# Kernel tuning notes

Hardware: AMD Instinct MI355X
Metric: run time of the kernel (lower is better)

## Reference

```python
import jax, jax.numpy as jnp
import numpy as np

T, B, D, H, DH = 2048, 2, 1024, 16, 64


def _rel_shift(x):
    # x: (Q, R, B, H) -- standard Transformer-XL relative shift via pad/reshape
    Q, R = x.shape[0], x.shape[1]
    zero_pad = jnp.zeros((Q, 1) + x.shape[2:], dtype=x.dtype)
    xp = jnp.concatenate([zero_pad, x], axis=1)          # (Q, R+1, B, H)
    xp = xp.reshape((R + 1, Q) + x.shape[2:])            # (R+1, Q, B, H)
    return xp[1:].reshape(x.shape)                       # (Q, R, B, H)


def setup_inputs() -> dict:
    key = jax.random.key(0)
    ks = jax.random.split(key, 7)
    w = jax.random.normal(ks[0], (T, B, D), dtype=jnp.float32)
    r = jax.random.normal(ks[1], (T, D), dtype=jnp.float32)
    w_qkv = jax.random.normal(ks[2], (3 * H * DH, D), dtype=jnp.float32) * 0.02
    w_r = jax.random.normal(ks[3], (H * DH, D), dtype=jnp.float32) * 0.02
    w_o = jax.random.normal(ks[4], (D, H * DH), dtype=jnp.float32) * 0.02
    r_r_bias = jax.random.normal(ks[5], (H, DH), dtype=jnp.float32) * 0.02
    attn_mask = jax.random.uniform(ks[6], (T, B)) < 0.1
    return {"w": w, "r": r, "w_qkv": w_qkv, "w_r": w_r, "w_o": w_o,
            "r_r_bias": r_r_bias, "attn_mask": attn_mask}


def reference(w, r, w_qkv, w_r, w_o, r_r_bias, attn_mask):
    qlen, bsz, d_model = w.shape
    n_head, d_head = r_r_bias.shape
    rlen = r.shape[0]
    scale = 1.0 / d_head ** 0.5

    heads = jnp.einsum('tbd,ed->tbe', w, w_qkv)           # (T, B, 3*H*DH)
    q, k, v = jnp.split(heads, 3, axis=-1)
    q = q.reshape(qlen, bsz, n_head, d_head)
    k = k.reshape(qlen, bsz, n_head, d_head)
    v = v.reshape(qlen, bsz, n_head, d_head)
    r_head_k = jnp.einsum('rd,ed->re', r, w_r).reshape(rlen, n_head, d_head)

    # NOTE: source uses r_r_bias for BOTH content and position biases
    rq = q + r_r_bias[None, None]                         # (Q, B, H, DH)
    AC = jnp.einsum('qbhd,kbhd->bhqk', rq, k)             # content scores
    BD = jnp.einsum('qbhd,rhd->bhqr', rq, r_head_k)       # position scores

    BD = jnp.transpose(BD, (2, 3, 0, 1))                  # (Q, R, B, H)
    BD = _rel_shift(BD)
    BD = jnp.transpose(BD, (2, 3, 0, 1))                  # (B, H, Q, R)
    BD = BD[:, :, :, :qlen]                               # klen == qlen

    score = (AC + BD) * scale                             # (B, H, Q, K)
    # key-padding mask (K, B) -> broadcast (B, 1, 1, K)
    score = jnp.where(attn_mask.T[:, None, None, :], -jnp.inf, score)

    prob = jax.nn.softmax(score.astype(jnp.float32), axis=-1).astype(score.dtype)
    attn_vec = jnp.einsum('bhqk,kbhd->qbhd', prob, v).reshape(qlen, bsz, n_head * d_head)
    out = jnp.einsum('qbe,de->qbd', attn_vec, w_o)        # (Q, B, D)
    return out, prob
```

## Files before the change

kernel.cpp:

```cpp
#include <hip/hip_runtime.h>
#include <hip/hip_bf16.h>
#include <cstdint>
#include <cstddef>

#define TLEN 2048
#define NB 2
#define DMODEL 1024
#define NH 16
#define NDH 64

typedef unsigned short ushortT;
typedef short bf16x8 __attribute__((ext_vector_type(8)));
typedef float f32x16 __attribute__((ext_vector_type(16)));

__device__ __forceinline__ ushortT f2bf(float f) {
  union { float f; unsigned int u; } x{f};
  unsigned int r = x.u + 0x7fff + ((x.u >> 16) & 1);
  return (ushortT)(r >> 16);
}
__device__ __forceinline__ unsigned int pk2(float lo, float hi) {
  return ((unsigned int)f2bf(hi) << 16) | (unsigned int)f2bf(lo);
}
__device__ __forceinline__ float bf2f(ushortT u) {
  union { unsigned int u; float f; } x;
  x.u = ((unsigned int)u) << 16;
  return x.f;
}

__device__ __forceinline__ void gld_lds16(const void* g, void* l) {
  __builtin_amdgcn_global_load_lds(
      (const __attribute__((address_space(1))) unsigned int*)g,
      (__attribute__((address_space(3))) unsigned int*)l, 16, 0, 0);
}


__global__ __launch_bounds__(256) void cvt_bf16(const float* __restrict__ in,
                                                ushortT* __restrict__ out, int n4) {
  int i = blockIdx.x * 256 + threadIdx.x;
  if (i < n4) {
    float4 v = reinterpret_cast<const float4*>(in)[i];
    ushort4 o;
    o.x = f2bf(v.x); o.y = f2bf(v.y); o.z = f2bf(v.z); o.w = f2bf(v.w);
    reinterpret_cast<ushort4*>(out)[i] = o;
  }
}

__global__ __launch_bounds__(256) void cvt_mask(const int* __restrict__ mask,
                                                float* __restrict__ mfl) {
  int j = blockIdx.x * 256 + threadIdx.x;
  if (j < TLEN) {
    mfl[j]        = mask[j * NB]     ? 0.f : 1.f;
    mfl[TLEN + j] = mask[j * NB + 1] ? 0.f : 1.f;
  }
}

__global__ __launch_bounds__(256) void zero_rkext(ushortT* __restrict__ rkE) {
  int i = threadIdx.x;
  int h = i >> 4, c = i & 15;
  ushort4 z; z.x = 0; z.y = 0; z.z = 0; z.w = 0;
  *reinterpret_cast<ushort4*>(rkE + ((size_t)h * 4096 + 2048) * NDH + c * 4) = z;
}


template <typename Epi>
__global__ __launch_bounds__(256) void gemm_bf16(const ushortT* __restrict__ A,
                                                 const ushortT* __restrict__ B,
                                                 int K, Epi epi) {
  __shared__ ushortT Al[128 * 64];
  __shared__ ushortT Bl[128 * 64];
  const int tid = threadIdx.x;
  const int lane = tid & 63;
  const int wv = tid >> 6;
  const int wm = wv >> 1, wn = wv & 1;
  const int m0 = blockIdx.y * 128;
  const int n0 = blockIdx.x * 128;
  const int r32 = lane & 31;
  const int hh = lane >> 5;

  f32x16 acc[2][2];
#pragma unroll
  for (int i = 0; i < 2; ++i)
#pragma unroll
    for (int j = 0; j < 2; ++j)
#pragma unroll
      for (int e = 0; e < 16; ++e) acc[i][j][e] = 0.f;

  for (int k0 = 0; k0 < K; k0 += 64) {
#pragma unroll
    for (int it = 0; it < 4; ++it) {
      int idx = it * 256 + tid;
      int r = idx >> 3, c = idx & 7;
      int gcol = k0 + ((c ^ (r & 7)) << 3);
      gld_lds16(A + (size_t)(m0 + r) * K + gcol, Al + idx * 8);
      gld_lds16(B + (size_t)(n0 + r) * K + gcol, Bl + idx * 8);
    }
    asm volatile("s_waitcnt vmcnt(0)");
    __syncthreads();
#pragma unroll
    for (int kc = 0; kc < 4; ++kc) {
      int lc = kc * 2 + hh;
      bf16x8 af[2], bfr[2];
#pragma unroll
      for (int f = 0; f < 2; ++f) {
        int ar = wm * 64 + f * 32 + r32;
        af[f] = *(const bf16x8*)(Al + ar * 64 + ((lc ^ (ar & 7)) << 3));
        int br = wn * 64 + f * 32 + r32;
        bfr[f] = *(const bf16x8*)(Bl + br * 64 + ((lc ^ (br & 7)) << 3));
      }
#pragma unroll
      for (int i = 0; i < 2; ++i)
#pragma unroll
        for (int j = 0; j < 2; ++j)
          acc[i][j] = __builtin_amdgcn_mfma_f32_32x32x16_bf16(af[i], bfr[j],
                                                              acc[i][j], 0, 0, 0);
    }
    __syncthreads();
  }

#pragma unroll
  for (int i = 0; i < 2; ++i)
#pragma unroll
    for (int j = 0; j < 2; ++j)
#pragma unroll
      for (int rg = 0; rg < 16; ++rg) {
        int m = m0 + wm * 64 + i * 32 + (rg & 3) + 8 * (rg >> 2) + 4 * hh;
        int n = n0 + wn * 64 + j * 32 + r32;
        epi.store(m, n, acc[i][j][rg]);
      }
}

struct EpiQKV {
  ushortT* qb; ushortT* kb; ushortT* vtb; const float* bias;
  __device__ void store(int m, int n, float val) const {
    int t = m >> 1, b = m & 1;
    int which = n >> 10;
    int h = (n >> 6) & (NH - 1);
    int dh = n & (NDH - 1);
    int bh = b * NH + h;
    if (which == 0)
      qb[((size_t)bh * TLEN + t) * NDH + dh] = f2bf(val + bias[(h << 6) | dh]);
    else if (which == 1)
      kb[((size_t)bh * TLEN + t) * NDH + dh] = f2bf(val);
    else
      vtb[((size_t)bh * NDH + dh) * TLEN + t] = f2bf(val);
  }
};

struct EpiRK {
  ushortT* rkE;
  __device__ void store(int m, int n, float val) const {
    int h = n >> 6, dh = n & 63;
    ushortT v = f2bf(val);
    rkE[((size_t)h * 4096 + m) * NDH + dh] = v;
    if (m <= 2046)
      rkE[((size_t)h * 4096 + m + 2049) * NDH + dh] = v;
  }
};

struct EpiOut {
  float* out;
  __device__ void store(int m, int n, float val) const {
    out[(size_t)m * DMODEL + n] = val;
  }
};


__global__ __launch_bounds__(128) void attn_fast(
    const ushortT* __restrict__ qb, const ushortT* __restrict__ kb,
    const ushortT* __restrict__ vtb, const ushortT* __restrict__ rkE,
    const float* __restrict__ mfl, unsigned int* __restrict__ S,
    float* __restrict__ linv_g, ushortT* __restrict__ av_bf) {
  __shared__ float W[2][64][32];
  __shared__ ushortT KT[2048];
  __shared__ ushortT VT[2048];
  __shared__ ushortT RK[6144];

  const int bh = blockIdx.y;
  const int b = bh >> 4, h = bh & 15;
  const int t = threadIdx.x >> 6;
  const int lane = threadIdx.x & 63;
  const int ql = lane & 31;
  const int hh = lane >> 5;
  const int Q0 = blockIdx.x * 64;
  const int q0 = Q0 + 32 * t;
  const int qg = q0 + ql;

  const ushortT* Qbh = qb + (size_t)bh * TLEN * NDH;
  const ushortT* Kbh = kb + (size_t)bh * TLEN * NDH;
  const ushortT* Vbh = vtb + (size_t)bh * NDH * TLEN;
  const ushortT* Rh  = rkE + (size_t)h * 4096 * NDH;
  const float* mflb  = mfl + (size_t)b * TLEN;
  unsigned int* Sb   = S + (size_t)bh * (TLEN / 2) * TLEN;
  float (*Wp)[32] = W[t];

  bf16x8 Qf[4], Qs[4];
  {
    int r2 = min(qg + 1, TLEN - 1);
#pragma unroll
    for (int c = 0; c < 4; ++c) {
      Qf[c] = *(const bf16x8*)(Qbh + (size_t)qg * NDH + c * 16 + hh * 8);
      Qs[c] = *(const bf16x8*)(Qbh + (size_t)r2 * NDH + c * 16 + hh * 8);
    }
  }

  f32x16 pacc0, pacc1;
#pragma unroll
  for (int i = 0; i < 16; ++i) { pacc0[i] = 0.f; pacc1[i] = 0.f; }
  float l_acc = 0.f;

  for (int j0 = 0; j0 < TLEN; j0 += 32) {
    __syncthreads();
    const int U = 1984 + j0 - Q0;
#pragma unroll
    for (int i = 0; i < 6; ++i) {
      int ci = (t * 6 + i) * 64 + lane;
      int row = ci >> 3, c = ci & 7;
      gld_lds16(Rh + (size_t)(U + row) * NDH + ((c ^ (row & 7)) << 3), RK + ci * 8);
    }
#pragma unroll
    for (int i = 0; i < 2; ++i) {
      int ci = (t * 2 + i) * 64 + lane;
      int row = ci >> 3, c = ci & 7;
      gld_lds16(Kbh + (size_t)(j0 + row) * NDH + ((c ^ (row & 7)) << 3), KT + ci * 8);
      int d = ci >> 2, c2 = ci & 3;
      gld_lds16(Vbh + (size_t)d * TLEN + j0 + ((c2 ^ (d & 3)) << 3), VT + ci * 8);
    }
    float4 mf4[4];
#pragma unroll
    for (int g = 0; g < 4; ++g)
      mf4[g] = *(const float4*)(mflb + j0 + 8 * g + 4 * hh);
    asm volatile("s_waitcnt vmcnt(0)");
    __syncthreads();

    const bool t0w1 = (j0 <= q0);
    const bool t1w1 = (j0 < q0);
    const int R1 = 32 * (1 - t) + ql;
    const int R2 = R1 + 32;

    f32x16 facc;
#pragma unroll
    for (int i = 0; i < 16; ++i) facc[i] = 0.f;
    __builtin_amdgcn_s_setprio(1);
#pragma unroll
    for (int c = 0; c < 4; ++c) {
      bf16x8 a = *(const bf16x8*)(RK + R1 * NDH + (((2 * c + hh) ^ (R1 & 7)) << 3));
      facc = __builtin_amdgcn_mfma_f32_32x32x16_bf16(a, t0w1 ? Qf[c] : Qs[c], facc, 0, 0, 0);
    }
    __builtin_amdgcn_s_setprio(0);
#pragma unroll
    for (int r = 0; r < 16; ++r)
      Wp[(r & 3) + 8 * (r >> 2) + 4 * hh][ql] = facc[r];

#pragma unroll
    for (int i = 0; i < 16; ++i) facc[i] = 0.f;
    __builtin_amdgcn_s_setprio(1);
#pragma unroll
    for (int c = 0; c < 4; ++c) {
      bf16x8 a = *(const bf16x8*)(RK + R2 * NDH + (((2 * c + hh) ^ (R2 & 7)) << 3));
      facc = __builtin_amdgcn_mfma_f32_32x32x16_bf16(a, t1w1 ? Qf[c] : Qs[c], facc, 0, 0, 0);
    }
    __builtin_amdgcn_s_setprio(0);
#pragma unroll
    for (int r = 0; r < 16; ++r)
      Wp[32 + (r & 3) + 8 * (r >> 2) + 4 * hh][ql] = facc[r];

    f32x16 cacc;
#pragma unroll
    for (int i = 0; i < 16; ++i) cacc[i] = 0.f;
    __builtin_amdgcn_s_setprio(1);
#pragma unroll
    for (int c = 0; c < 4; ++c) {
      bf16x8 a = *(const bf16x8*)(KT + ql * NDH + (((2 * c + hh) ^ (ql & 7)) << 3));
      cacc = __builtin_amdgcn_mfma_f32_32x32x16_bf16(a, Qf[c], cacc, 0, 0, 0);
    }
    __builtin_amdgcn_s_setprio(0);

    float p[16];
#pragma unroll
    for (int r = 0; r < 16; ++r) {
      int jrow = (r & 3) + 8 * (r >> 2) + 4 * hh;
      float bd = Wp[jrow - ql + 31][ql];
      float sc = (cacc[r] + bd) * 0.125f;
      float mv = (&mf4[r >> 2].x)[r & 3];
      float pv = mv * __expf(sc);
      p[r] = pv;
      l_acc += pv;
    }

    unsigned int u[8];
#pragma unroll
    for (int i = 0; i < 8; ++i) u[i] = pk2(p[2 * i], p[2 * i + 1]);

#pragma unroll
    for (int i = 0; i < 8; ++i) {
      int r = 2 * i;
      int jrow = (r & 3) + 8 * (r >> 2) + 4 * hh;
      Sb[(size_t)((j0 + jrow) >> 1) * TLEN + qg] = u[i];
    }

#pragma unroll
    for (int kh = 0; kh < 2; ++kh) {
      unsigned int t0 = (unsigned int)__shfl_xor((int)u[4 * kh + 0], 32);
      unsigned int t1 = (unsigned int)__shfl_xor((int)u[4 * kh + 1], 32);
      unsigned int t2 = (unsigned int)__shfl_xor((int)u[4 * kh + 2], 32);
      unsigned int t3 = (unsigned int)__shfl_xor((int)u[4 * kh + 3], 32);
      unsigned int fr[4];
      fr[0] = hh ? t2 : u[4 * kh + 0];
      fr[1] = hh ? t3 : u[4 * kh + 1];
      fr[2] = hh ? u[4 * kh + 2] : t0;
      fr[3] = hh ? u[4 * kh + 3] : t1;
      bf16x8 pa = *reinterpret_cast<bf16x8*>(fr);
      bf16x8 v0 = *(const bf16x8*)(VT + ql * 32 + (((2 * kh + hh) ^ (ql & 3)) << 3));
      bf16x8 v1 = *(const bf16x8*)(VT + (32 + ql) * 32 + (((2 * kh + hh) ^ (ql & 3)) << 3));
      __builtin_amdgcn_s_setprio(1);
      pacc0 = __builtin_amdgcn_mfma_f32_32x32x16_bf16(pa, v0, pacc0, 0, 0, 0);
      pacc1 = __builtin_amdgcn_mfma_f32_32x32x16_bf16(pa, v1, pacc1, 0, 0, 0);
      __builtin_amdgcn_s_setprio(0);
    }
  }

  float lt = l_acc + __shfl_xor(l_acc, 32);
  if (lane < 32) linv_g[(size_t)bh * TLEN + qg] = 1.0f / lt;
  float inv = 1.0f / lt;
#pragma unroll
  for (int r = 0; r < 16; ++r) {
    int qrow = (r & 3) + 8 * (r >> 2) + 4 * hh;
    float iv = __shfl(inv, qrow);
    size_t aoff = ((size_t)(q0 + qrow) * NB + b) * DMODEL + h * NDH;
    av_bf[aoff + ql] = f2bf(pacc0[r] * iv);
    av_bf[aoff + 32 + ql] = f2bf(pacc1[r] * iv);
  }
}


__global__ __launch_bounds__(256) void rescale_t(const unsigned int* __restrict__ S,
                                                 const float* __restrict__ linv_g,
                                                 float* __restrict__ prob) {
  __shared__ unsigned int lds[64][65];
  __shared__ float liv[64];
  const int qt = blockIdx.x;
  const int jt = blockIdx.y;
  const int bh = blockIdx.z;
  const int t = threadIdx.x;

  const unsigned int* Sb = S + ((size_t)bh * (TLEN / 2) + jt * 64) * TLEN + qt * 64;
  {
    int row = t >> 2, c0 = (t & 3) * 16;
#pragma unroll
    for (int k = 0; k < 4; ++k) {
      uint4 v = *reinterpret_cast<const uint4*>(Sb + (size_t)row * TLEN + c0 + k * 4);
      lds[row][c0 + k * 4 + 0] = v.x;
      lds[row][c0 + k * 4 + 1] = v.y;
      lds[row][c0 + k * 4 + 2] = v.z;
      lds[row][c0 + k * 4 + 3] = v.w;
    }
  }
  if (t < 64) liv[t] = linv_g[(size_t)bh * TLEN + qt * 64 + t];
  __syncthreads();

  float* P = prob + ((size_t)bh * TLEN + qt * 64) * TLEN + jt * 128;
#pragma unroll
  for (int k = 0; k < 8; ++k) {
    int idx = k * 256 + t;
    int row = idx >> 5, c4 = idx & 31;
    unsigned int u0 = lds[c4 * 2][row];
    unsigned int u1 = lds[c4 * 2 + 1][row];
    float iv = liv[row];
    float4 o;
    o.x = bf2f((ushortT)(u0 & 0xffff)) * iv;
    o.y = bf2f((ushortT)(u0 >> 16)) * iv;
    o.z = bf2f((ushortT)(u1 & 0xffff)) * iv;
    o.w = bf2f((ushortT)(u1 >> 16)) * iv;
    *reinterpret_cast<float4*>(P + (size_t)row * TLEN + c4 * 4) = o;
  }
}


__global__ __launch_bounds__(256) void attn_fused(
    const ushortT* __restrict__ qb, const ushortT* __restrict__ kb,
    const ushortT* __restrict__ vtb, const ushortT* __restrict__ rkE,
    const float* __restrict__ mfl, float* __restrict__ prob,
    ushortT* __restrict__ av_bf) {
  __shared__ float W[4][64][32];
  __shared__ float sl[4][32];
  __shared__ float linv[64];

  const int bh = blockIdx.y;
  const int b = bh >> 4, h = bh & 15;
  const int wv = threadIdx.x >> 6;
  const int lane = threadIdx.x & 63;
  const int ql = lane & 31;
  const int hh = lane >> 5;
  const int qtile = wv & 1;
  const int jh = wv >> 1;
  const int q0 = blockIdx.x * 64 + qtile * 32;
  const int qg = q0 + ql;

  const ushortT* Qbh = qb + (size_t)bh * TLEN * NDH;
  const ushortT* Kbh = kb + (size_t)bh * TLEN * NDH;
  const ushortT* Vbh = vtb + (size_t)bh * NDH * TLEN;
  const ushortT* Rh  = rkE + (size_t)h * 4096 * NDH;
  const float* mflb  = mfl + (size_t)b * TLEN;
  float (*Wp)[32] = W[wv];

  bf16x8 Qf[4], Qs[4];
  {
    int r2 = min(qg + 1, TLEN - 1);
#pragma unroll
    for (int c = 0; c < 4; ++c) {
      Qf[c] = *(const bf16x8*)(Qbh + (size_t)qg * NDH + c * 16 + hh * 8);
      Qs[c] = *(const bf16x8*)(Qbh + (size_t)r2 * NDH + c * 16 + hh * 8);
    }
  }

  f32x16 pacc0, pacc1;
#pragma unroll
  for (int i = 0; i < 16; ++i) { pacc0[i] = 0.f; pacc1[i] = 0.f; }
  float l_acc = 0.f;

  ushortT* pbrow = (ushortT*)prob + ((size_t)bh * TLEN + qg) * 4096 + 2048;

  const int jbeg = jh * (TLEN / 2);
  const int jend = jbeg + (TLEN / 2);
  for (int j0 = jbeg; j0 < jend; j0 += 32) {
    const int base_t = 2016 + j0 - q0;
    const bool t0w1 = (j0 <= q0);
    const bool t1w1 = (j0 < q0);

    const ushortT* s0 = Rh + (size_t)(base_t + ql) * NDH + hh * 8;
    const ushortT* s1 = Rh + (size_t)(base_t + 32 + ql) * NDH + hh * 8;
    const ushortT* sk = Kbh + (size_t)(j0 + ql) * NDH + hh * 8;
    const ushortT* vrow0 = Vbh + (size_t)ql * TLEN + j0 + 8 * hh;
    const ushortT* vrow1 = Vbh + (size_t)(32 + ql) * TLEN + j0 + 8 * hh;
    bf16x8 rk0[4], rk1[4], kk[4];
#pragma unroll
    for (int c = 0; c < 4; ++c) {
      rk0[c] = *(const bf16x8*)(s0 + c * 16);
      rk1[c] = *(const bf16x8*)(s1 + c * 16);
      kk[c]  = *(const bf16x8*)(sk + c * 16);
    }
    bf16x8 v00 = *(const bf16x8*)(vrow0);
    bf16x8 v01 = *(const bf16x8*)(vrow0 + 16);
    bf16x8 v10 = *(const bf16x8*)(vrow1);
    bf16x8 v11 = *(const bf16x8*)(vrow1 + 16);
    float4 mf4[4];
#pragma unroll
    for (int g = 0; g < 4; ++g)
      mf4[g] = *(const float4*)(mflb + j0 + 8 * g + 4 * hh);

    f32x16 facc;
#pragma unroll
    for (int i = 0; i < 16; ++i) facc[i] = 0.f;
    __builtin_amdgcn_s_setprio(1);
#pragma unroll
    for (int c = 0; c < 4; ++c)
      facc = __builtin_amdgcn_mfma_f32_32x32x16_bf16(rk0[c], t0w1 ? Qf[c] : Qs[c], facc, 0, 0, 0);
    __builtin_amdgcn_s_setprio(0);
#pragma unroll
    for (int r = 0; r < 16; ++r)
      Wp[(r & 3) + 8 * (r >> 2) + 4 * hh][ql] = facc[r];

#pragma unroll
    for (int i = 0; i < 16; ++i) facc[i] = 0.f;
    __builtin_amdgcn_s_setprio(1);
#pragma unroll
    for (int c = 0; c < 4; ++c)
      facc = __builtin_amdgcn_mfma_f32_32x32x16_bf16(rk1[c], t1w1 ? Qf[c] : Qs[c], facc, 0, 0, 0);
    __builtin_amdgcn_s_setprio(0);
#pragma unroll
    for (int r = 0; r < 16; ++r)
      Wp[32 + (r & 3) + 8 * (r >> 2) + 4 * hh][ql] = facc[r];

    f32x16 cacc;
#pragma unroll
    for (int i = 0; i < 16; ++i) cacc[i] = 0.f;
    __builtin_amdgcn_s_setprio(1);
#pragma unroll
    for (int c = 0; c < 4; ++c)
      cacc = __builtin_amdgcn_mfma_f32_32x32x16_bf16(kk[c], Qf[c], cacc, 0, 0, 0);
    __builtin_amdgcn_s_setprio(0);

    float p[16];
#pragma unroll
    for (int r = 0; r < 16; ++r) {
      int jrow = (r & 3) + 8 * (r >> 2) + 4 * hh;
      float bd = Wp[jrow - ql + 31][ql];
      float sc = (cacc[r] + bd) * 0.125f;
      float mv = (&mf4[r >> 2].x)[r & 3];
      float pv = mv * __expf(sc);
      p[r] = pv;
      l_acc += pv;
    }

#pragma unroll
    for (int g = 0; g < 4; ++g) {
      uint2 st;
      st.x = pk2(p[4 * g + 0], p[4 * g + 1]);
      st.y = pk2(p[4 * g + 2], p[4 * g + 3]);
      *reinterpret_cast<uint2*>(pbrow + j0 + 8 * g + 4 * hh) = st;
    }

#pragma unroll
    for (int kh = 0; kh < 2; ++kh) {
      unsigned int u0 = pk2(p[8 * kh + 0], p[8 * kh + 1]);
      unsigned int u1 = pk2(p[8 * kh + 2], p[8 * kh + 3]);
      unsigned int u2 = pk2(p[8 * kh + 4], p[8 * kh + 5]);
      unsigned int u3 = pk2(p[8 * kh + 6], p[8 * kh + 7]);
      unsigned int t0 = (unsigned int)__shfl_xor((int)u0, 32);
      unsigned int t1 = (unsigned int)__shfl_xor((int)u1, 32);
      unsigned int t2 = (unsigned int)__shfl_xor((int)u2, 32);
      unsigned int t3 = (unsigned int)__shfl_xor((int)u3, 32);
      unsigned int fr[4];
      fr[0] = hh ? t2 : u0;
      fr[1] = hh ? t3 : u1;
      fr[2] = hh ? u2 : t0;
      fr[3] = hh ? u3 : t1;
      bf16x8 pa = *reinterpret_cast<bf16x8*>(fr);
      __builtin_amdgcn_s_setprio(1);
      pacc0 = __builtin_amdgcn_mfma_f32_32x32x16_bf16(pa, kh ? v01 : v00, pacc0, 0, 0, 0);
      pacc1 = __builtin_amdgcn_mfma_f32_32x32x16_bf16(pa, kh ? v11 : v10, pacc1, 0, 0, 0);
      __builtin_amdgcn_s_setprio(0);
    }
  }

#pragma unroll
  for (int r = 0; r < 16; ++r) {
    int qrow = (r & 3) + 8 * (r >> 2) + 4 * hh;
    Wp[qrow][ql] = pacc0[r];
    Wp[32 + qrow][ql] = pacc1[r];
  }
  float lh = l_acc + __shfl_xor(l_acc, 32);
  if (lane < 32) sl[wv][ql] = lh;
  __syncthreads();

  if (wv < 2) {
    if (lane < 32) {
      float lt = sl[wv][ql] + sl[wv + 2][ql];
      linv[wv * 32 + ql] = 1.0f / lt;
    }
#pragma unroll
    for (int r = 0; r < 16; ++r) {
      int qrow = (r & 3) + 8 * (r >> 2) + 4 * hh;
      float lt = sl[wv][qrow] + sl[wv + 2][qrow];
      float iv = 1.0f / lt;
      float s0v = W[wv][qrow][ql] + W[wv + 2][qrow][ql];
      float s1v = W[wv][32 + qrow][ql] + W[wv + 2][32 + qrow][ql];
      size_t aoff = ((size_t)(q0 + qrow) * NB + b) * DMODEL + h * NDH;
      av_bf[aoff + ql] = f2bf(s0v * iv);
      av_bf[aoff + 32 + ql] = f2bf(s1v * iv);
    }
  }
  __syncthreads();

  const ushortT* probus = (const ushortT*)prob;
  const int lr = lane >> 4;
  const int cg = lane & 15;
  for (int s = 0; s < 8; ++s) {
    const int rloc = qtile * 32 + s * 4 + lr;
    const int rowg = blockIdx.x * 64 + rloc;
    const size_t ub = ((size_t)bh * TLEN + rowg) * 4096 + 2048 + jh * 1024 + cg * 8;
    const size_t fb = ((size_t)bh * TLEN + rowg) * 2048 + jh * 1024 + cg * 8;
    uint4 a[8];
#pragma unroll
    for (int k = 0; k < 8; ++k)
      a[k] = *reinterpret_cast<const uint4*>(probus + ub + k * 128);
    const float iv = linv[rloc];
    __syncthreads();
#pragma unroll
    for (int k = 0; k < 8; ++k) {
      float4 o0, o1;
      o0.x = bf2f((ushortT)(a[k].x & 0xffff)) * iv;
      o0.y = bf2f((ushortT)(a[k].x >> 16)) * iv;
      o0.z = bf2f((ushortT)(a[k].y & 0xffff)) * iv;
      o0.w = bf2f((ushortT)(a[k].y >> 16)) * iv;
      o1.x = bf2f((ushortT)(a[k].z & 0xffff)) * iv;
      o1.y = bf2f((ushortT)(a[k].z >> 16)) * iv;
      o1.z = bf2f((ushortT)(a[k].w & 0xffff)) * iv;
      o1.w = bf2f((ushortT)(a[k].w >> 16)) * iv;
      *reinterpret_cast<float4*>(prob + fb + k * 128) = o0;
      *reinterpret_cast<float4*>(prob + fb + k * 128 + 4) = o1;
    }
  }
}


extern "C" void kernel_launch(void* const* d_in, const int* in_sizes, int n_in,
                              void* d_out, int out_size, void* d_ws, size_t ws_size,
                              hipStream_t stream) {
  const float* w      = (const float*)d_in[0];
  const float* r      = (const float*)d_in[1];
  const float* w_qkv  = (const float*)d_in[2];
  const float* w_r    = (const float*)d_in[3];
  const float* w_o    = (const float*)d_in[4];
  const float* bias   = (const float*)d_in[5];
  const int* mask     = (const int*)d_in[6];

  float* out  = (float*)d_out;
  float* prob = out + (size_t)TLEN * NB * DMODEL;

  const size_t SZ = (size_t)NB * NH * TLEN * NDH;
  ushortT* w_bf    = (ushortT*)d_ws;
  ushortT* wqkv_bf = w_bf + (size_t)4096 * 1024;
  ushortT* r_bf    = wqkv_bf + (size_t)3072 * 1024;
  ushortT* wr_bf   = r_bf + (size_t)2048 * 1024;
  ushortT* wo_bf   = wr_bf + (size_t)1024 * 1024;
  ushortT* q_bf    = wo_bf + (size_t)1024 * 1024;
  ushortT* k_bf    = q_bf + SZ;
  ushortT* vt_bf   = k_bf + SZ;
  ushortT* rkE_bf  = vt_bf + SZ;
  ushortT* av_bf   = rkE_bf + (size_t)NH * 4096 * NDH;
  float* mfl       = (float*)(av_bf + SZ);
  float* linv_g    = mfl + (size_t)NB * TLEN;
  unsigned int* S  = (unsigned int*)(linv_g + (size_t)NB * NH * TLEN);
  const size_t need = (size_t)((char*)(S + (size_t)NB * NH * (TLEN / 2) * TLEN) -
                               (char*)d_ws);
  const bool fast = ws_size >= need;

  cvt_bf16<<<4096, 256, 0, stream>>>(w, w_bf, 4096 * 1024 / 4);
  cvt_bf16<<<3072, 256, 0, stream>>>(w_qkv, wqkv_bf, 3072 * 1024 / 4);
  cvt_bf16<<<2048, 256, 0, stream>>>(r, r_bf, 2048 * 1024 / 4);
  cvt_bf16<<<1024, 256, 0, stream>>>(w_r, wr_bf, 1024 * 1024 / 4);
  cvt_bf16<<<1024, 256, 0, stream>>>(w_o, wo_bf, 1024 * 1024 / 4);
  cvt_mask<<<8, 256, 0, stream>>>(mask, mfl);
  zero_rkext<<<1, 256, 0, stream>>>(rkE_bf);

  EpiQKV e1{q_bf, k_bf, vt_bf, bias};
  gemm_bf16<EpiQKV><<<dim3(3072 / 128, 4096 / 128), 256, 0, stream>>>(w_bf, wqkv_bf, DMODEL, e1);
  EpiRK e2{rkE_bf};
  gemm_bf16<EpiRK><<<dim3(1024 / 128, 2048 / 128), 256, 0, stream>>>(r_bf, wr_bf, DMODEL, e2);

  if (fast) {
    attn_fast<<<dim3(32, 32), 128, 0, stream>>>(q_bf, k_bf, vt_bf, rkE_bf,
                                                mfl, S, linv_g, av_bf);
    rescale_t<<<dim3(32, 16, 32), 256, 0, stream>>>(S, linv_g, prob);
  } else {
    attn_fused<<<dim3(32, 32), 256, 0, stream>>>(q_bf, k_bf, vt_bf, rkE_bf,
                                                 mfl, prob, av_bf);
  }

  EpiOut e5{out};
  gemm_bf16<EpiOut><<<dim3(1024 / 128, 4096 / 128), 256, 0, stream>>>(av_bf, wo_bf, DMODEL, e5);
}
```

Baseline: 471.3 us.

## Prefetch next attention tile during compute and merge conversion kernels into one launch

The attention loop now pulls all LDS operands for the current tile into registers, then issues the async global-to-LDS loads for the next tile before running the MFMAs, so load latency overlaps compute. It uses a single LDS buffer and relies on barriers and a partial vmcnt wait to keep the two phases apart. Separately, the five bf16 conversion kernels plus the mask and zero-fill kernels are folded into one launch to cut launch overhead. The register-held operands raise register pressure, and a wrong wait count could race on the shared buffers.

New measurement: 445.4 us (median of 2 runs). 5.5% less time.

```diff
diff --git a/kernel.cpp b/kernel.cpp
--- a/kernel.cpp
+++ b/kernel.cpp
@@ -34,31 +34,43 @@
 }
 
 
-__global__ __launch_bounds__(256) void cvt_bf16(const float* __restrict__ in,
-                                                ushortT* __restrict__ out, int n4) {
-  int i = blockIdx.x * 256 + threadIdx.x;
-  if (i < n4) {
-    float4 v = reinterpret_cast<const float4*>(in)[i];
-    ushort4 o;
-    o.x = f2bf(v.x); o.y = f2bf(v.y); o.z = f2bf(v.z); o.w = f2bf(v.w);
-    reinterpret_cast<ushort4*>(out)[i] = o;
-  }
-}
-
-__global__ __launch_bounds__(256) void cvt_mask(const int* __restrict__ mask,
-                                                float* __restrict__ mfl) {
-  int j = blockIdx.x * 256 + threadIdx.x;
-  if (j < TLEN) {
-    mfl[j]        = mask[j * NB]     ? 0.f : 1.f;
-    mfl[TLEN + j] = mask[j * NB + 1] ? 0.f : 1.f;
-  }
-}
-
-__global__ __launch_bounds__(256) void zero_rkext(ushortT* __restrict__ rkE) {
-  int i = threadIdx.x;
-  int h = i >> 4, c = i & 15;
-  ushort4 z; z.x = 0; z.y = 0; z.z = 0; z.w = 0;
-  *reinterpret_cast<ushort4*>(rkE + ((size_t)h * 4096 + 2048) * NDH + c * 4) = z;
+__global__ __launch_bounds__(256) void cvt_all(
+    const float* __restrict__ w, const float* __restrict__ wqkv,
+    const float* __restrict__ r, const float* __restrict__ wr,
+    const float* __restrict__ wo, ushortT* __restrict__ w_bf,
+    ushortT* __restrict__ wqkv_bf, ushortT* __restrict__ r_bf,
+    ushortT* __restrict__ wr_bf, ushortT* __restrict__ wo_bf,
+    const int* __restrict__ mask, float* __restrict__ mfl,
+    ushortT* __restrict__ rkE) {
+  const size_t N0 = 1048576, N1 = N0 + 786432, N2 = N1 + 524288,
+               N3 = N2 + 262144, N4 = N3 + 262144;
+  size_t i = (size_t)blockIdx.x * 256 + threadIdx.x;
+  const float* src; ushortT* dst; size_t off;
+  if (i < N0)      { src = w;    dst = w_bf;    off = i; }
+  else if (i < N1) { src = wqkv; dst = wqkv_bf; off = i - N0; }
+  else if (i < N2) { src = r;    dst = r_bf;    off = i - N1; }
+  else if (i < N3) { src = wr;   dst = wr_bf;   off = i - N2; }
+  else if (i < N4) { src = wo;   dst = wo_bf;   off = i - N3; }
+  else {
+    size_t k = i - N4;
+    if (k < 512) {
+      int j = (int)k * 4;
+#pragma unroll
+      for (int s = 0; s < 4; ++s) {
+        mfl[j + s]        = mask[(size_t)(j + s) * NB]     ? 0.f : 1.f;
+        mfl[TLEN + j + s] = mask[(size_t)(j + s) * NB + 1] ? 0.f : 1.f;
+      }
+    } else if (k < 512 + 256) {
+      int ii = (int)k - 512; int h = ii >> 4, c = ii & 15;
+      ushort4 z; z.x = 0; z.y = 0; z.z = 0; z.w = 0;
+      *reinterpret_cast<ushort4*>(rkE + ((size_t)h * 4096 + 2048) * NDH + c * 4) = z;
+    }
+    return;
+  }
+  float4 v = reinterpret_cast<const float4*>(src)[off];
+  ushort4 o;
+  o.x = f2bf(v.x); o.y = f2bf(v.y); o.z = f2bf(v.z); o.w = f2bf(v.w);
+  reinterpret_cast<ushort4*>(dst)[off] = o;
 }
 
 
@@ -193,23 +205,7 @@
   unsigned int* Sb   = S + (size_t)bh * (TLEN / 2) * TLEN;
   float (*Wp)[32] = W[t];
 
-  bf16x8 Qf[4], Qs[4];
-  {
-    int r2 = min(qg + 1, TLEN - 1);
-#pragma unroll
-    for (int c = 0; c < 4; ++c) {
-      Qf[c] = *(const bf16x8*)(Qbh + (size_t)qg * NDH + c * 16 + hh * 8);
-      Qs[c] = *(const bf16x8*)(Qbh + (size_t)r2 * NDH + c * 16 + hh * 8);
-    }
-  }
-
-  f32x16 pacc0, pacc1;
-#pragma unroll
-  for (int i = 0; i < 16; ++i) { pacc0[i] = 0.f; pacc1[i] = 0.f; }
-  float l_acc = 0.f;
-
-  for (int j0 = 0; j0 < TLEN; j0 += 32) {
-    __syncthreads();
+  auto STAGE = [&](int j0) {
     const int U = 1984 + j0 - Q0;
 #pragma unroll
     for (int i = 0; i < 6; ++i) {
@@ -225,27 +221,63 @@
       int d = ci >> 2, c2 = ci & 3;
       gld_lds16(Vbh + (size_t)d * TLEN + j0 + ((c2 ^ (d & 3)) << 3), VT + ci * 8);
     }
+  };
+
+  bf16x8 Qf[4], Qs[4];
+  {
+    int r2 = min(qg + 1, TLEN - 1);
+#pragma unroll
+    for (int c = 0; c < 4; ++c) {
+      Qf[c] = *(const bf16x8*)(Qbh + (size_t)qg * NDH + c * 16 + hh * 8);
+      Qs[c] = *(const bf16x8*)(Qbh + (size_t)r2 * NDH + c * 16 + hh * 8);
+    }
+  }
+
+  f32x16 pacc0, pacc1;
+#pragma unroll
+  for (int i = 0; i < 16; ++i) { pacc0[i] = 0.f; pacc1[i] = 0.f; }
+  float l_acc = 0.f;
+
+  STAGE(0);
+  asm volatile("s_waitcnt vmcnt(0)");
+  __builtin_amdgcn_s_barrier();
+
+  for (int j0 = 0; j0 < TLEN; j0 += 32) {
     float4 mf4[4];
 #pragma unroll
     for (int g = 0; g < 4; ++g)
       mf4[g] = *(const float4*)(mflb + j0 + 8 * g + 4 * hh);
-    asm volatile("s_waitcnt vmcnt(0)");
-    __syncthreads();
+
+    const int R1 = 32 * (1 - t) + ql;
+    const int R2 = R1 + 32;
+    bf16x8 a1[4], a2[4], ak[4];
+#pragma unroll
+    for (int c = 0; c < 4; ++c) {
+      a1[c] = *(const bf16x8*)(RK + R1 * 64 + (((2 * c + hh) ^ (R1 & 7)) << 3));
+      a2[c] = *(const bf16x8*)(RK + R2 * 64 + (((2 * c + hh) ^ (R2 & 7)) << 3));
+      ak[c] = *(const bf16x8*)(KT + ql * 64 + (((2 * c + hh) ^ (ql & 7)) << 3));
+    }
+    bf16x8 vv0[2], vv1[2];
+#pragma unroll
+    for (int kh = 0; kh < 2; ++kh) {
+      vv0[kh] = *(const bf16x8*)(VT + ql * 32 + (((2 * kh + hh) ^ (ql & 3)) << 3));
+      vv1[kh] = *(const bf16x8*)(VT + (32 + ql) * 32 + (((2 * kh + hh) ^ (ql & 3)) << 3));
+    }
+    asm volatile("s_waitcnt lgkmcnt(0)");
+    __builtin_amdgcn_s_barrier();
+
+    if (j0 + 32 < TLEN) STAGE(j0 + 32);
 
     const bool t0w1 = (j0 <= q0);
     const bool t1w1 = (j0 < q0);
-    const int R1 = 32 * (1 - t) + ql;
-    const int R2 = R1 + 32;
 
     f32x16 facc;
 #pragma unroll
     for (int i = 0; i < 16; ++i) facc[i] = 0.f;
     __builtin_amdgcn_s_setprio(1);
 #pragma unroll
-    for (int c = 0; c < 4; ++c) {
-      bf16x8 a = *(const bf16x8*)(RK + R1 * NDH + (((2 * c + hh) ^ (R1 & 7)) << 3));
-      facc = __builtin_amdgcn_mfma_f32_32x32x16_bf16(a, t0w1 ? Qf[c] : Qs[c], facc, 0, 0, 0);
-    }
+    for (int c = 0; c < 4; ++c)
+      facc = __builtin_amdgcn_mfma_f32_32x32x16_bf16(a1[c], t0w1 ? Qf[c] : Qs[c], facc, 0, 0, 0);
     __builtin_amdgcn_s_setprio(0);
 #pragma unroll
     for (int r = 0; r < 16; ++r)
@@ -255,10 +287,8 @@
     for (int i = 0; i < 16; ++i) facc[i] = 0.f;
     __builtin_amdgcn_s_setprio(1);
 #pragma unroll
-    for (int c = 0; c < 4; ++c) {
-      bf16x8 a = *(const bf16x8*)(RK + R2 * NDH + (((2 * c + hh) ^ (R2 & 7)) << 3));
-      facc = __builtin_amdgcn_mfma_f32_32x32x16_bf16(a, t1w1 ? Qf[c] : Qs[c], facc, 0, 0, 0);
-    }
+    for (int c = 0; c < 4; ++c)
+      facc = __builtin_amdgcn_mfma_f32_32x32x16_bf16(a2[c], t1w1 ? Qf[c] : Qs[c], facc, 0, 0, 0);
     __builtin_amdgcn_s_setprio(0);
 #pragma unroll
     for (int r = 0; r < 16; ++r)
@@ -269,10 +299,8 @@
     for (int i = 0; i < 16; ++i) cacc[i] = 0.f;
     __builtin_amdgcn_s_setprio(1);
 #pragma unroll
-    for (int c = 0; c < 4; ++c) {
-      bf16x8 a = *(const bf16x8*)(KT + ql * NDH + (((2 * c + hh) ^ (ql & 7)) << 3));
-      cacc = __builtin_amdgcn_mfma_f32_32x32x16_bf16(a, Qf[c], cacc, 0, 0, 0);
-    }
+    for (int c = 0; c < 4; ++c)
+      cacc = __builtin_amdgcn_mfma_f32_32x32x16_bf16(ak[c], Qf[c], cacc, 0, 0, 0);
     __builtin_amdgcn_s_setprio(0);
 
     float p[16];
@@ -310,12 +338,15 @@
       fr[2] = hh ? u[4 * kh + 2] : t0;
       fr[3] = hh ? u[4 * kh + 3] : t1;
       bf16x8 pa = *reinterpret_cast<bf16x8*>(fr);
-      bf16x8 v0 = *(const bf16x8*)(VT + ql * 32 + (((2 * kh + hh) ^ (ql & 3)) << 3));
-      bf16x8 v1 = *(const bf16x8*)(VT + (32 + ql) * 32 + (((2 * kh + hh) ^ (ql & 3)) << 3));
       __builtin_amdgcn_s_setprio(1);
-      pacc0 = __builtin_amdgcn_mfma_f32_32x32x16_bf16(pa, v0, pacc0, 0, 0, 0);
-      pacc1 = __builtin_amdgcn_mfma_f32_32x32x16_bf16(pa, v1, pacc1, 0, 0, 0);
+      pacc0 = __builtin_amdgcn_mfma_f32_32x32x16_bf16(pa, kh ? vv0[1] : vv0[0], pacc0, 0, 0, 0);
+      pacc1 = __builtin_amdgcn_mfma_f32_32x32x16_bf16(pa, kh ? vv1[1] : vv1[0], pacc1, 0, 0, 0);
       __builtin_amdgcn_s_setprio(0);
+    }
+
+    if (j0 + 32 < TLEN) {
+      asm volatile("s_waitcnt vmcnt(8)");
+      __builtin_amdgcn_s_barrier();
     }
   }
 
@@ -616,13 +647,8 @@
                                (char*)d_ws);
   const bool fast = ws_size >= need;
 
-  cvt_bf16<<<4096, 256, 0, stream>>>(w, w_bf, 4096 * 1024 / 4);
-  cvt_bf16<<<3072, 256, 0, stream>>>(w_qkv, wqkv_bf, 3072 * 1024 / 4);
-  cvt_bf16<<<2048, 256, 0, stream>>>(r, r_bf, 2048 * 1024 / 4);
-  cvt_bf16<<<1024, 256, 0, stream>>>(w_r, wr_bf, 1024 * 1024 / 4);
-  cvt_bf16<<<1024, 256, 0, stream>>>(w_o, wo_bf, 1024 * 1024 / 4);
-  cvt_mask<<<8, 256, 0, stream>>>(mask, mfl);
-  zero_rkext<<<1, 256, 0, stream>>>(rkE_bf);
+  cvt_all<<<dim3((2883584 + 768 + 255) / 256), 256, 0, stream>>>(
+      w, w_qkv, r, w_r, w_o, w_bf, wqkv_bf, r_bf, wr_bf, wo_bf, mask, mfl, rkE_bf);
 
   EpiQKV e1{q_bf, k_bf, vt_bf, bias};
   gemm_bf16<EpiQKV><<<dim3(3072 / 128, 4096 / 128), 256, 0, stream>>>(w_bf, wqkv_bf, DMODEL, e1);
```
